# Performance work log

Hardware: AMD Instinct MI355X
Metric: run time of the kernel (lower is better)

## Reference

```python
import jax, jax.numpy as jnp
import numpy as np

N = 10000
E = 640000


def setup_inputs() -> dict:
    key = jax.random.key(0)
    k = jax.random.split(key, 6)
    x = jax.random.normal(k[0], (N, 128), dtype=jnp.float32)
    edge_index = jax.random.randint(k[1], (2, E), 0, N, dtype=jnp.int64)
    # Linear weights stored as [in, out] (torch stores [out, in]; math is x @ W.T + b)
    w1 = jax.random.normal(k[2], (128, 128), dtype=jnp.float32) * 0.05
    b1 = jax.random.normal(k[3], (128,), dtype=jnp.float32) * 0.05
    w2 = jax.random.normal(k[4], (128, 128), dtype=jnp.float32) * 0.05
    b2 = jax.random.normal(k[5], (128,), dtype=jnp.float32) * 0.05
    return {"x": x, "edge_index": edge_index, "w1": w1, "b1": b1, "w2": w2, "b2": b2}


def gin_conv(x, src, dst, w, b, eps=0.0):
    # aggregate: out[i] = sum over edges (src->dst=i) of x[src]
    agg = jax.ops.segment_sum(x[src], dst, num_segments=N)  # [N, d]
    h = (1.0 + eps) * x + agg
    return h @ w + b


def reference(x, edge_index, w1, b1, w2, b2):
    src, dst = edge_index[0], edge_index[1]
    h = gin_conv(x, src, dst, w1, b1)
    h = jax.nn.relu(h)
    h = gin_conv(h, src, dst, w2, b2)
    return jax.nn.log_softmax(h, axis=1)
```

## Files before the change

### kernel.cpp

```cpp
#include <hip/hip_runtime.h>
#include <cstdint>

#define NNODES 10000
#define FDIM 128
#define MAXDEG 192
#define SLOTS 48

typedef _Float16 h2v  __attribute__((ext_vector_type(2)));
typedef _Float16 f16x8 __attribute__((ext_vector_type(8)));
typedef float    f32x4 __attribute__((ext_vector_type(4)));

__device__ __align__(16)  int      g_cnt[NNODES * 4];
__device__                int      g_bucket[NNODES * MAXDEG];
__device__ __align__(256) unsigned g_xh [(NNODES + 1) * FDIM / 2];
__device__ __align__(256) unsigned g_h1h[(NNODES + 1) * FDIM / 2];
__device__ __align__(16)  unsigned g_wf[2 * 8192];

__device__ inline h2v as_h2(unsigned u) { return __builtin_bit_cast(h2v, u); }
__device__ inline unsigned as_u(h2v v) { return __builtin_bit_cast(unsigned, v); }
__device__ inline unsigned pack_f16x2(float a, float b) {
  h2v v; v[0] = (_Float16)a; v[1] = (_Float16)b;
  return as_u(v);
}
__device__ inline void vadd4(uint4& a, const uint4& b) {
  a.x = as_u(as_h2(a.x) + as_h2(b.x));
  a.y = as_u(as_h2(a.y) + as_h2(b.y));
  a.z = as_u(as_h2(a.z) + as_h2(b.z));
  a.w = as_u(as_h2(a.w) + as_h2(b.w));
}

__global__ __launch_bounds__(256) void prep_kernel(
    const float* __restrict__ x, const int* __restrict__ ei,
    const float* __restrict__ w1, const float* __restrict__ w2,
    int E_, int EBLK, int CBLK) {
  const int bid = blockIdx.x;
  if (bid < EBLK) {
    int e = bid * 256 + threadIdx.x;
    if (e < E_) {
      int d = ei[E_ + e];
      int s = ei[e];
      int st = e & 3;
      int p = atomicAdd(&g_cnt[d * 4 + st], 1);
      if (p < SLOTS) g_bucket[d * MAXDEG + st * SLOTS + p] = s;
    }
  } else if (bid < EBLK + CBLK) {
    int i = (bid - EBLK) * 256 + threadIdx.x;
    if (i < NNODES * 32) {
      float4 v = *(const float4*)(x + 4 * (size_t)i);
      uint2 o; o.x = pack_f16x2(v.x, v.y); o.y = pack_f16x2(v.z, v.w);
      *(uint2*)(g_xh + 2 * (size_t)i) = o;
    }
  } else {
    int idx = (bid - EBLK - CBLK) * 256 + threadIdx.x;
    const float* w = (idx >= 2048) ? w2 : w1;
    int s = idx & 2047;
    int sl = s & 63, nk = s >> 6;
    int n = nk >> 2, kc = nk & 3;
    int kbase = kc * 32 + (sl >> 4) * 8;
    int f = n * 16 + (sl & 15);
    unsigned d0 = pack_f16x2(w[(size_t)(kbase + 0) * FDIM + f],
                             w[(size_t)(kbase + 1) * FDIM + f]);
    unsigned d1 = pack_f16x2(w[(size_t)(kbase + 2) * FDIM + f],
                             w[(size_t)(kbase + 3) * FDIM + f]);
    unsigned d2 = pack_f16x2(w[(size_t)(kbase + 4) * FDIM + f],
                             w[(size_t)(kbase + 5) * FDIM + f]);
    unsigned d3 = pack_f16x2(w[(size_t)(kbase + 6) * FDIM + f],
                             w[(size_t)(kbase + 7) * FDIM + f]);
    *(uint4*)(g_wf + (idx >> 11) * 8192 + 4 * s) = make_uint4(d0, d1, d2, d3);
  }
}

template <int MODE>
__global__ __launch_bounds__(512) void gin_layer_kernel(
    const float* __restrict__ bvec,
    float* __restrict__ out_g) {
  const unsigned* __restrict__ xh = (MODE == 0) ? g_xh : g_h1h;

  __shared__ __align__(16) unsigned al[16 * 68];
  __shared__ __align__(16) unsigned cfu[8 * 132];

  const int tid = threadIdx.x;
  const int wave = tid >> 6, lane = tid & 63;
  const int quad = lane >> 4, m16 = lane & 15;
  const int node0 = blockIdx.x * 8;
  const int myn = node0 + wave;

  uint4 bf[4];
  {
    const unsigned* wfp = g_wf + (MODE ? 8192 : 0);
#pragma unroll
    for (int kc = 0; kc < 4; ++kc)
      bf[kc] = *(const uint4*)(wfp + ((wave * 4 + kc) * 64 + lane) * 4);
  }
  const float bb = bvec[wave * 16 + m16];

  for (int i2 = tid; i2 < 8 * 68; i2 += 512) al[8 * 68 + i2] = 0;

  uint4 self4 = *(const uint4*)(xh + (size_t)myn * 64 + (m16 << 2));
  int o1, o2, o3, deg;
  {
    int4 c = *(const int4*)(g_cnt + myn * 4);
    int a = (c.x > SLOTS) ? SLOTS : c.x;
    int bq = (c.y > SLOTS) ? SLOTS : c.y;
    int cq = (c.z > SLOTS) ? SLOTS : c.z;
    int dq = (c.w > SLOTS) ? SLOTS : c.w;
    o1 = a; o2 = a + bq; o3 = a + bq + cq; deg = a + bq + cq + dq;
  }

  const int* nb = g_bucket + (size_t)myn * MAXDEG;
  int idxr[3];
#pragma unroll
  for (int r = 0; r < 3; ++r) {
    int g = r * 64 + lane;
    int e = NNODES;
    if (g < deg) {
      int base = 0;
      if (g >= o1) base = o1;
      if (g >= o2) base = o2;
      if (g >= o3) base = o3;
      int st = (g >= o1) + (g >= o2) + (g >= o3);
      e = nb[st * SLOTS + (g - base)];
    }
    idxr[r] = e;
  }

  h2v a0 = as_h2(0u), a1 = as_h2(0u), a2 = as_h2(0u), a3 = as_h2(0u);
  const int nbat = (deg + 31) >> 5;
  for (int bt = 0; bt < nbat; ++bt) {
    const int s0 = bt << 3;
    const int r = s0 >> 4;
    const int src = (r == 0) ? idxr[0] : ((r == 1) ? idxr[1] : idxr[2]);
    uint4 t[8];
#pragma unroll
    for (int k = 0; k < 8; ++k) {
      int e = __builtin_amdgcn_ds_bpermute(
          (((((s0 + k) & 15) << 2) | quad) << 2), src);
      t[k] = *(const uint4*)(xh + (unsigned)((e << 6) | (m16 << 2)));
    }
#pragma unroll
    for (int st2 = 1; st2 < 8; st2 <<= 1)
#pragma unroll
      for (int k = 0; k < 8; k += 2 * st2) vadd4(t[k], t[k + st2]);
    a0 += as_h2(t[0].x); a1 += as_h2(t[0].y);
    a2 += as_h2(t[0].z); a3 += as_h2(t[0].w);
  }

  int rr;
  rr = __shfl_xor((int)as_u(a0), 16, 64); a0 += as_h2((unsigned)rr);
  rr = __shfl_xor((int)as_u(a0), 32, 64); a0 += as_h2((unsigned)rr);
  rr = __shfl_xor((int)as_u(a1), 16, 64); a1 += as_h2((unsigned)rr);
  rr = __shfl_xor((int)as_u(a1), 32, 64); a1 += as_h2((unsigned)rr);
  rr = __shfl_xor((int)as_u(a2), 16, 64); a2 += as_h2((unsigned)rr);
  rr = __shfl_xor((int)as_u(a2), 32, 64); a2 += as_h2((unsigned)rr);
  rr = __shfl_xor((int)as_u(a3), 16, 64); a3 += as_h2((unsigned)rr);
  rr = __shfl_xor((int)as_u(a3), 32, 64); a3 += as_h2((unsigned)rr);
  a0 += as_h2(self4.x); a1 += as_h2(self4.y);
  a2 += as_h2(self4.z); a3 += as_h2(self4.w);
  if (quad == 0)
    *(uint4*)(al + wave * 68 + (m16 << 2)) =
        make_uint4(as_u(a0), as_u(a1), as_u(a2), as_u(a3));
  __syncthreads();

  uint4 af[4];
#pragma unroll
  for (int kc = 0; kc < 4; ++kc)
    af[kc] = *(const uint4*)(al + m16 * 68 + kc * 16 + quad * 4);

  const int n = wave;
  f32x4 acc = {0.f, 0.f, 0.f, 0.f};
#pragma unroll
  for (int kc = 0; kc < 4; ++kc)
    acc = __builtin_amdgcn_mfma_f32_16x16x32_f16(
            __builtin_bit_cast(f16x8, af[kc]),
            __builtin_bit_cast(f16x8, bf[kc]), acc, 0, 0, 0);

  if (MODE == 0) {
    _Float16* ch = (_Float16*)cfu;
    const int f = n * 16 + m16;
    if (quad < 2) {
#pragma unroll
      for (int reg = 0; reg < 4; ++reg)
        ch[(quad * 4 + reg) * 136 + f] = (_Float16)fmaxf(acc[reg] + bb, 0.f);
    }
    __syncthreads();
    if (tid < 256) {
      const int row = tid >> 5, c2 = (tid & 31) * 2;
      uint2 v = *(const uint2*)(cfu + row * 68 + c2);
      *(uint2*)(&g_h1h[(size_t)(node0 + row) * 64 + c2]) = v;
    }
  } else {
    float* cf = (float*)cfu;
    const int f = n * 16 + m16;
    if (quad < 2) {
#pragma unroll
      for (int reg = 0; reg < 4; ++reg)
        cf[(quad * 4 + reg) * 132 + f] = acc[reg] + bb;
    }
    __syncthreads();
    if (tid < 256) {
      const int row = tid >> 5, li = tid & 31;
      const float* base = cf + row * 132 + li * 4;
      float4 a4 = *(const float4*)(base);
      float mx = fmaxf(fmaxf(a4.x, a4.y), fmaxf(a4.z, a4.w));
#pragma unroll
      for (int off = 16; off >= 1; off >>= 1)
        mx = fmaxf(mx, __shfl_xor(mx, off, 64));
      float s = (__expf(a4.x - mx) + __expf(a4.y - mx))
              + (__expf(a4.z - mx) + __expf(a4.w - mx));
#pragma unroll
      for (int off = 16; off >= 1; off >>= 1)
        s += __shfl_xor(s, off, 64);
      const float ls = mx + __logf(s);
      float* orow = out_g + (size_t)(node0 + row) * FDIM + li * 4;
      *(float4*)(orow) = make_float4(a4.x - ls, a4.y - ls, a4.z - ls, a4.w - ls);
    }
    if (tid < 32) g_cnt[node0 * 4 + tid] = 0;
  }
}

extern "C" void kernel_launch(void* const* d_in, const int* in_sizes, int n_in,
                              void* d_out, int out_size, void* d_ws, size_t ws_size,
                              hipStream_t stream) {
  const float* x  = (const float*)d_in[0];
  const int*   ei = (const int*)d_in[1];
  const float* w1 = (const float*)d_in[2];
  const float* b1 = (const float*)d_in[3];
  const float* w2 = (const float*)d_in[4];
  const float* b2 = (const float*)d_in[5];
  float* out = (float*)d_out;

  const int E_ = in_sizes[1] / 2;
  const int EBLK = (E_ + 255) / 256;
  const int CBLK = (NNODES * 32 + 255) / 256;
  const int WBLK = 16;

  prep_kernel<<<EBLK + CBLK + WBLK, 256, 0, stream>>>(x, ei, w1, w2, E_, EBLK, CBLK);

  gin_layer_kernel<0><<<1250, 512, 0, stream>>>(b1, nullptr);
  gin_layer_kernel<1><<<1250, 512, 0, stream>>>(b2, out);
}
```

Before: 124.2 us.

## Use one wave per 8-node block and pad counter stride to reduce atomic contention

New measurement: 142.1 us. +14.4%, slower.

```diff
diff --git a/kernel.cpp b/kernel.cpp
--- a/kernel.cpp
+++ b/kernel.cpp
@@ -5,12 +5,13 @@
 #define FDIM 128
 #define MAXDEG 192
 #define SLOTS 48
+#define CSTRIDE 16
 
 typedef _Float16 h2v  __attribute__((ext_vector_type(2)));
 typedef _Float16 f16x8 __attribute__((ext_vector_type(8)));
 typedef float    f32x4 __attribute__((ext_vector_type(4)));
 
-__device__ __align__(16)  int      g_cnt[NNODES * 4];
+__device__ __align__(16)  int      g_cnt[NNODES * CSTRIDE];
 __device__                int      g_bucket[NNODES * MAXDEG];
 __device__ __align__(256) unsigned g_xh [(NNODES + 1) * FDIM / 2];
 __device__ __align__(256) unsigned g_h1h[(NNODES + 1) * FDIM / 2];
@@ -40,7 +41,7 @@
       int d = ei[E_ + e];
       int s = ei[e];
       int st = e & 3;
-      int p = atomicAdd(&g_cnt[d * 4 + st], 1);
+      int p = atomicAdd(&g_cnt[d * CSTRIDE + st], 1);
       if (p < SLOTS) g_bucket[d * MAXDEG + st * SLOTS + p] = s;
     }
   } else if (bid < EBLK + CBLK) {
@@ -71,150 +72,179 @@
 }
 
 template <int MODE>
-__global__ __launch_bounds__(512) void gin_layer_kernel(
+__global__ __launch_bounds__(64) void gin_layer_kernel(
     const float* __restrict__ bvec,
     float* __restrict__ out_g) {
   const unsigned* __restrict__ xh = (MODE == 0) ? g_xh : g_h1h;
 
-  __shared__ __align__(16) unsigned al[16 * 68];
-  __shared__ __align__(16) unsigned cfu[8 * 132];
-
-  const int tid = threadIdx.x;
-  const int wave = tid >> 6, lane = tid & 63;
+  __shared__ __align__(16) unsigned buf[16 * 68];
+
+  const int lane = threadIdx.x;
   const int quad = lane >> 4, m16 = lane & 15;
   const int node0 = blockIdx.x * 8;
-  const int myn = node0 + wave;
-
-  uint4 bf[4];
-  {
-    const unsigned* wfp = g_wf + (MODE ? 8192 : 0);
-#pragma unroll
-    for (int kc = 0; kc < 4; ++kc)
-      bf[kc] = *(const uint4*)(wfp + ((wave * 4 + kc) * 64 + lane) * 4);
-  }
-  const float bb = bvec[wave * 16 + m16];
-
-  for (int i2 = tid; i2 < 8 * 68; i2 += 512) al[8 * 68 + i2] = 0;
-
-  uint4 self4 = *(const uint4*)(xh + (size_t)myn * 64 + (m16 << 2));
-  int o1, o2, o3, deg;
-  {
-    int4 c = *(const int4*)(g_cnt + myn * 4);
+
+  for (int i2 = lane; i2 < 8 * 68; i2 += 64) buf[8 * 68 + i2] = 0;
+
+  int4 cnxt = *(const int4*)(g_cnt + (size_t)node0 * CSTRIDE);
+  for (int nd = 0; nd < 8; ++nd) {
+    const int myn = node0 + nd;
+    int4 c = cnxt;
+    if (nd < 7)
+      cnxt = *(const int4*)(g_cnt + (size_t)(myn + 1) * CSTRIDE);
     int a = (c.x > SLOTS) ? SLOTS : c.x;
     int bq = (c.y > SLOTS) ? SLOTS : c.y;
     int cq = (c.z > SLOTS) ? SLOTS : c.z;
     int dq = (c.w > SLOTS) ? SLOTS : c.w;
-    o1 = a; o2 = a + bq; o3 = a + bq + cq; deg = a + bq + cq + dq;
-  }
-
-  const int* nb = g_bucket + (size_t)myn * MAXDEG;
-  int idxr[3];
-#pragma unroll
-  for (int r = 0; r < 3; ++r) {
-    int g = r * 64 + lane;
-    int e = NNODES;
-    if (g < deg) {
-      int base = 0;
-      if (g >= o1) base = o1;
-      if (g >= o2) base = o2;
-      if (g >= o3) base = o3;
-      int st = (g >= o1) + (g >= o2) + (g >= o3);
-      e = nb[st * SLOTS + (g - base)];
-    }
-    idxr[r] = e;
-  }
-
-  h2v a0 = as_h2(0u), a1 = as_h2(0u), a2 = as_h2(0u), a3 = as_h2(0u);
-  const int nbat = (deg + 31) >> 5;
-  for (int bt = 0; bt < nbat; ++bt) {
-    const int s0 = bt << 3;
-    const int r = s0 >> 4;
-    const int src = (r == 0) ? idxr[0] : ((r == 1) ? idxr[1] : idxr[2]);
-    uint4 t[8];
-#pragma unroll
-    for (int k = 0; k < 8; ++k) {
-      int e = __builtin_amdgcn_ds_bpermute(
-          (((((s0 + k) & 15) << 2) | quad) << 2), src);
-      t[k] = *(const uint4*)(xh + (unsigned)((e << 6) | (m16 << 2)));
-    }
-#pragma unroll
-    for (int st2 = 1; st2 < 8; st2 <<= 1)
-#pragma unroll
-      for (int k = 0; k < 8; k += 2 * st2) vadd4(t[k], t[k + st2]);
-    a0 += as_h2(t[0].x); a1 += as_h2(t[0].y);
-    a2 += as_h2(t[0].z); a3 += as_h2(t[0].w);
-  }
-
-  int rr;
-  rr = __shfl_xor((int)as_u(a0), 16, 64); a0 += as_h2((unsigned)rr);
-  rr = __shfl_xor((int)as_u(a0), 32, 64); a0 += as_h2((unsigned)rr);
-  rr = __shfl_xor((int)as_u(a1), 16, 64); a1 += as_h2((unsigned)rr);
-  rr = __shfl_xor((int)as_u(a1), 32, 64); a1 += as_h2((unsigned)rr);
-  rr = __shfl_xor((int)as_u(a2), 16, 64); a2 += as_h2((unsigned)rr);
-  rr = __shfl_xor((int)as_u(a2), 32, 64); a2 += as_h2((unsigned)rr);
-  rr = __shfl_xor((int)as_u(a3), 16, 64); a3 += as_h2((unsigned)rr);
-  rr = __shfl_xor((int)as_u(a3), 32, 64); a3 += as_h2((unsigned)rr);
-  a0 += as_h2(self4.x); a1 += as_h2(self4.y);
-  a2 += as_h2(self4.z); a3 += as_h2(self4.w);
-  if (quad == 0)
-    *(uint4*)(al + wave * 68 + (m16 << 2)) =
-        make_uint4(as_u(a0), as_u(a1), as_u(a2), as_u(a3));
+    const int o1 = a, o2 = a + bq, o3 = a + bq + cq;
+    const int deg = a + bq + cq + dq;
+
+    const int* nb = g_bucket + (size_t)myn * MAXDEG;
+    int i0 = NNODES, i1 = NNODES, i2r = NNODES;
+    {
+      int g = lane;
+      if (g < deg) {
+        int base = 0;
+        if (g >= o1) base = o1;
+        if (g >= o2) base = o2;
+        if (g >= o3) base = o3;
+        int st = (g >= o1) + (g >= o2) + (g >= o3);
+        i0 = nb[st * SLOTS + (g - base)];
+      }
+      g = 64 + lane;
+      if (g < deg) {
+        int base = 0;
+        if (g >= o1) base = o1;
+        if (g >= o2) base = o2;
+        if (g >= o3) base = o3;
+        int st = (g >= o1) + (g >= o2) + (g >= o3);
+        i1 = nb[st * SLOTS + (g - base)];
+      }
+      g = 128 + lane;
+      if (g < deg) {
+        int base = 0;
+        if (g >= o1) base = o1;
+        if (g >= o2) base = o2;
+        if (g >= o3) base = o3;
+        int st = (g >= o1) + (g >= o2) + (g >= o3);
+        i2r = nb[st * SLOTS + (g - base)];
+      }
+    }
+
+    uint4 self4 = *(const uint4*)(xh + (size_t)myn * 64 + (m16 << 2));
+
+    h2v a0 = as_h2(0u), a1 = as_h2(0u), a2 = as_h2(0u), a3 = as_h2(0u);
+    const int nbat = (deg + 31) >> 5;
+    for (int bt = 0; bt < nbat; ++bt) {
+      const int r = bt >> 1;
+      const int src = (r == 0) ? i0 : ((r == 1) ? i1 : i2r);
+      const int base = (bt & 1) << 5;
+      uint4 t[8];
+#pragma unroll
+      for (int k = 0; k < 8; ++k) {
+        int e = __builtin_amdgcn_ds_bpermute((base + 4 * k + quad) << 2, src);
+        t[k] = *(const uint4*)(xh + (unsigned)((e << 6) | (m16 << 2)));
+      }
+#pragma unroll
+      for (int st2 = 1; st2 < 8; st2 <<= 1)
+#pragma unroll
+        for (int k = 0; k < 8; k += 2 * st2) vadd4(t[k], t[k + st2]);
+      a0 += as_h2(t[0].x); a1 += as_h2(t[0].y);
+      a2 += as_h2(t[0].z); a3 += as_h2(t[0].w);
+    }
+
+    int rr;
+    rr = __shfl_xor((int)as_u(a0), 16, 64); a0 += as_h2((unsigned)rr);
+    rr = __shfl_xor((int)as_u(a0), 32, 64); a0 += as_h2((unsigned)rr);
+    rr = __shfl_xor((int)as_u(a1), 16, 64); a1 += as_h2((unsigned)rr);
+    rr = __shfl_xor((int)as_u(a1), 32, 64); a1 += as_h2((unsigned)rr);
+    rr = __shfl_xor((int)as_u(a2), 16, 64); a2 += as_h2((unsigned)rr);
+    rr = __shfl_xor((int)as_u(a2), 32, 64); a2 += as_h2((unsigned)rr);
+    rr = __shfl_xor((int)as_u(a3), 16, 64); a3 += as_h2((unsigned)rr);
+    rr = __shfl_xor((int)as_u(a3), 32, 64); a3 += as_h2((unsigned)rr);
+    a0 += as_h2(self4.x); a1 += as_h2(self4.y);
+    a2 += as_h2(self4.z); a3 += as_h2(self4.w);
+    if (quad == 0)
+      *(uint4*)(buf + nd * 68 + (m16 << 2)) =
+          make_uint4(as_u(a0), as_u(a1), as_u(a2), as_u(a3));
+  }
   __syncthreads();
 
   uint4 af[4];
 #pragma unroll
   for (int kc = 0; kc < 4; ++kc)
-    af[kc] = *(const uint4*)(al + m16 * 68 + kc * 16 + quad * 4);
-
-  const int n = wave;
-  f32x4 acc = {0.f, 0.f, 0.f, 0.f};
-#pragma unroll
-  for (int kc = 0; kc < 4; ++kc)
-    acc = __builtin_amdgcn_mfma_f32_16x16x32_f16(
-            __builtin_bit_cast(f16x8, af[kc]),
-            __builtin_bit_cast(f16x8, bf[kc]), acc, 0, 0, 0);
+    af[kc] = *(const uint4*)(buf + m16 * 68 + kc * 16 + quad * 4);
+  __syncthreads();
+
+  const unsigned* wfp = g_wf + (MODE ? 8192 : 0);
+#pragma unroll
+  for (int n = 0; n < 8; ++n) {
+    f32x4 acc = {0.f, 0.f, 0.f, 0.f};
+#pragma unroll
+    for (int kc = 0; kc < 4; ++kc) {
+      uint4 bfr = *(const uint4*)(wfp + ((n * 4 + kc) * 64 + lane) * 4);
+      acc = __builtin_amdgcn_mfma_f32_16x16x32_f16(
+              __builtin_bit_cast(f16x8, af[kc]),
+              __builtin_bit_cast(f16x8, bfr), acc, 0, 0, 0);
+    }
+    const float bbn = bvec[n * 16 + m16];
+    if (MODE == 0) {
+      _Float16* ch = (_Float16*)buf;
+      const int f = n * 16 + m16;
+      if (quad < 2) {
+#pragma unroll
+        for (int reg = 0; reg < 4; ++reg)
+          ch[(quad * 4 + reg) * 136 + f] = (_Float16)fmaxf(acc[reg] + bbn, 0.f);
+      }
+    } else {
+      float* cf = (float*)buf;
+      const int f = n * 16 + m16;
+      if (quad < 2) {
+#pragma unroll
+        for (int reg = 0; reg < 4; ++reg)
+          cf[(quad * 4 + reg) * 132 + f] = acc[reg] + bbn;
+      }
+    }
+  }
+  __syncthreads();
 
   if (MODE == 0) {
-    _Float16* ch = (_Float16*)cfu;
-    const int f = n * 16 + m16;
-    if (quad < 2) {
-#pragma unroll
-      for (int reg = 0; reg < 4; ++reg)
-        ch[(quad * 4 + reg) * 136 + f] = (_Float16)fmaxf(acc[reg] + bb, 0.f);
-    }
-    __syncthreads();
-    if (tid < 256) {
-      const int row = tid >> 5, c2 = (tid & 31) * 2;
-      uint2 v = *(const uint2*)(cfu + row * 68 + c2);
+    const int row = lane >> 3;
+#pragma unroll
+    for (int j = 0; j < 4; ++j) {
+      const int c2 = (lane & 7) * 2 + j * 16;
+      uint2 v = *(const uint2*)(buf + row * 68 + c2);
       *(uint2*)(&g_h1h[(size_t)(node0 + row) * 64 + c2]) = v;
     }
   } else {
-    float* cf = (float*)cfu;
-    const int f = n * 16 + m16;
-    if (quad < 2) {
-#pragma unroll
-      for (int reg = 0; reg < 4; ++reg)
-        cf[(quad * 4 + reg) * 132 + f] = acc[reg] + bb;
-    }
-    __syncthreads();
-    if (tid < 256) {
-      const int row = tid >> 5, li = tid & 31;
-      const float* base = cf + row * 132 + li * 4;
-      float4 a4 = *(const float4*)(base);
-      float mx = fmaxf(fmaxf(a4.x, a4.y), fmaxf(a4.z, a4.w));
-#pragma unroll
-      for (int off = 16; off >= 1; off >>= 1)
-        mx = fmaxf(mx, __shfl_xor(mx, off, 64));
-      float s = (__expf(a4.x - mx) + __expf(a4.y - mx))
-              + (__expf(a4.z - mx) + __expf(a4.w - mx));
-#pragma unroll
-      for (int off = 16; off >= 1; off >>= 1)
-        s += __shfl_xor(s, off, 64);
-      const float ls = mx + __logf(s);
-      float* orow = out_g + (size_t)(node0 + row) * FDIM + li * 4;
-      *(float4*)(orow) = make_float4(a4.x - ls, a4.y - ls, a4.z - ls, a4.w - ls);
-    }
-    if (tid < 32) g_cnt[node0 * 4 + tid] = 0;
+    const float* cf = (const float*)buf;
+    const int row = lane >> 3, li = lane & 7;
+    const float* base = cf + row * 132 + li * 16;
+    float4 v[4];
+#pragma unroll
+    for (int jj = 0; jj < 4; ++jj) v[jj] = *(const float4*)(base + jj * 4);
+    float mx = -1e30f;
+#pragma unroll
+    for (int jj = 0; jj < 4; ++jj)
+      mx = fmaxf(mx, fmaxf(fmaxf(v[jj].x, v[jj].y), fmaxf(v[jj].z, v[jj].w)));
+#pragma unroll
+    for (int off = 4; off >= 1; off >>= 1)
+      mx = fmaxf(mx, __shfl_xor(mx, off, 64));
+    float s = 0.f;
+#pragma unroll
+    for (int jj = 0; jj < 4; ++jj)
+      s += (__expf(v[jj].x - mx) + __expf(v[jj].y - mx))
+         + (__expf(v[jj].z - mx) + __expf(v[jj].w - mx));
+#pragma unroll
+    for (int off = 4; off >= 1; off >>= 1)
+      s += __shfl_xor(s, off, 64);
+    const float ls = mx + __logf(s);
+    float* orow = out_g + (size_t)(node0 + row) * FDIM + li * 16;
+#pragma unroll
+    for (int jj = 0; jj < 4; ++jj)
+      *(float4*)(orow + jj * 4) =
+          make_float4(v[jj].x - ls, v[jj].y - ls, v[jj].z - ls, v[jj].w - ls);
+    if (lane < 32)
+      g_cnt[(node0 + (lane >> 2)) * CSTRIDE + (lane & 3)] = 0;
   }
 }
 
@@ -236,6 +266,6 @@
 
   prep_kernel<<<EBLK + CBLK + WBLK, 256, 0, stream>>>(x, ei, w1, w2, E_, EBLK, CBLK);
 
-  gin_layer_kernel<0><<<1250, 512, 0, stream>>>(b1, nullptr);
-  gin_layer_kernel<1><<<1250, 512, 0, stream>>>(b2, out);
-}
+  gin_layer_kernel<0><<<1250, 64, 0, stream>>>(b1, nullptr);
+  gin_layer_kernel<1><<<1250, 64, 0, stream>>>(b2, out);
+}
```

## Build adjacency buckets in shared memory per node range with 16-bit indices

Applied to the files above, without the earlier changes.

New measurement: 397.1 us. +219.7%, slower.

```diff
diff --git a/kernel.cpp b/kernel.cpp
--- a/kernel.cpp
+++ b/kernel.cpp
@@ -4,14 +4,15 @@
 #define NNODES 10000
 #define FDIM 128
 #define MAXDEG 192
-#define SLOTS 48
+#define NPB 157
+#define SCANBLK 64
 
 typedef _Float16 h2v  __attribute__((ext_vector_type(2)));
 typedef _Float16 f16x8 __attribute__((ext_vector_type(8)));
 typedef float    f32x4 __attribute__((ext_vector_type(4)));
 
-__device__ __align__(16)  int      g_cnt[NNODES * 4];
-__device__                int      g_bucket[NNODES * MAXDEG];
+__device__ __align__(16)  int            g_cnt[NNODES];
+__device__ __align__(16)  unsigned short g_bkt[NNODES * MAXDEG];
 __device__ __align__(256) unsigned g_xh [(NNODES + 1) * FDIM / 2];
 __device__ __align__(256) unsigned g_h1h[(NNODES + 1) * FDIM / 2];
 __device__ __align__(16)  unsigned g_wf[2 * 8192];
@@ -29,44 +30,73 @@
   a.w = as_u(as_h2(a.w) + as_h2(b.w));
 }
 
-__global__ __launch_bounds__(256) void prep_kernel(
+__global__ __launch_bounds__(512) void prep_kernel(
     const float* __restrict__ x, const int* __restrict__ ei,
     const float* __restrict__ w1, const float* __restrict__ w2,
-    int E_, int EBLK, int CBLK) {
-  const int bid = blockIdx.x;
-  if (bid < EBLK) {
-    int e = bid * 256 + threadIdx.x;
-    if (e < E_) {
-      int d = ei[E_ + e];
-      int s = ei[e];
-      int st = e & 3;
-      int p = atomicAdd(&g_cnt[d * 4 + st], 1);
-      if (p < SLOTS) g_bucket[d * MAXDEG + st * SLOTS + p] = s;
-    }
-  } else if (bid < EBLK + CBLK) {
-    int i = (bid - EBLK) * 256 + threadIdx.x;
+    int E_) {
+  __shared__ int lcnt[NPB];
+  __shared__ __align__(16) unsigned short lbkt[NPB * MAXDEG];
+
+  const int bid = blockIdx.x, tid = threadIdx.x;
+  if (bid < SCANBLK) {
+    const int lo = bid * NPB;
+    const int nn = (NNODES - lo < NPB) ? (NNODES - lo) : NPB;
+    for (int i = tid; i < NPB; i += 512) lcnt[i] = 0;
+    __syncthreads();
+
+    const int iters = (E_ + 511) >> 9;
+    for (int it = 0; it < iters; it += 8) {
+      int dv[8];
+#pragma unroll
+      for (int k = 0; k < 8; ++k) {
+        int e = (it + k) * 512 + tid;
+        dv[k] = (e < E_) ? ei[E_ + e] : -1;
+      }
+#pragma unroll
+      for (int k = 0; k < 8; ++k) {
+        unsigned rel = (unsigned)(dv[k] - lo);
+        if (rel < (unsigned)nn) {
+          int e = (it + k) * 512 + tid;
+          int s = ei[e];
+          int p = atomicAdd(&lcnt[rel], 1);
+          if (p < MAXDEG) lbkt[rel * MAXDEG + p] = (unsigned short)s;
+        }
+      }
+    }
+    __syncthreads();
+
+    for (int i = tid; i < nn; i += 512)
+      g_cnt[lo + i] = (lcnt[i] > MAXDEG) ? MAXDEG : lcnt[i];
+    const int nq = nn * (MAXDEG * 2 / 16);
+    const uint4* srcq = (const uint4*)lbkt;
+    uint4* dstq = (uint4*)(g_bkt + (size_t)lo * MAXDEG);
+    for (int i = tid; i < nq; i += 512) dstq[i] = srcq[i];
+  } else if (bid < SCANBLK + 625) {
+    int i = (bid - SCANBLK) * 512 + tid;
     if (i < NNODES * 32) {
       float4 v = *(const float4*)(x + 4 * (size_t)i);
       uint2 o; o.x = pack_f16x2(v.x, v.y); o.y = pack_f16x2(v.z, v.w);
       *(uint2*)(g_xh + 2 * (size_t)i) = o;
     }
   } else {
-    int idx = (bid - EBLK - CBLK) * 256 + threadIdx.x;
-    const float* w = (idx >= 2048) ? w2 : w1;
-    int s = idx & 2047;
-    int sl = s & 63, nk = s >> 6;
-    int n = nk >> 2, kc = nk & 3;
-    int kbase = kc * 32 + (sl >> 4) * 8;
-    int f = n * 16 + (sl & 15);
-    unsigned d0 = pack_f16x2(w[(size_t)(kbase + 0) * FDIM + f],
-                             w[(size_t)(kbase + 1) * FDIM + f]);
-    unsigned d1 = pack_f16x2(w[(size_t)(kbase + 2) * FDIM + f],
-                             w[(size_t)(kbase + 3) * FDIM + f]);
-    unsigned d2 = pack_f16x2(w[(size_t)(kbase + 4) * FDIM + f],
-                             w[(size_t)(kbase + 5) * FDIM + f]);
-    unsigned d3 = pack_f16x2(w[(size_t)(kbase + 6) * FDIM + f],
-                             w[(size_t)(kbase + 7) * FDIM + f]);
-    *(uint4*)(g_wf + (idx >> 11) * 8192 + 4 * s) = make_uint4(d0, d1, d2, d3);
+    int idx = (bid - SCANBLK - 625) * 512 + tid;
+    if (idx < 4096) {
+      const float* w = (idx >= 2048) ? w2 : w1;
+      int s = idx & 2047;
+      int sl = s & 63, nk = s >> 6;
+      int n = nk >> 2, kc = nk & 3;
+      int kbase = kc * 32 + (sl >> 4) * 8;
+      int f = n * 16 + (sl & 15);
+      unsigned d0 = pack_f16x2(w[(size_t)(kbase + 0) * FDIM + f],
+                               w[(size_t)(kbase + 1) * FDIM + f]);
+      unsigned d1 = pack_f16x2(w[(size_t)(kbase + 2) * FDIM + f],
+                               w[(size_t)(kbase + 3) * FDIM + f]);
+      unsigned d2 = pack_f16x2(w[(size_t)(kbase + 4) * FDIM + f],
+                               w[(size_t)(kbase + 5) * FDIM + f]);
+      unsigned d3 = pack_f16x2(w[(size_t)(kbase + 6) * FDIM + f],
+                               w[(size_t)(kbase + 7) * FDIM + f]);
+      *(uint4*)(g_wf + (idx >> 11) * 8192 + 4 * s) = make_uint4(d0, d1, d2, d3);
+    }
   }
 }
 
@@ -97,44 +127,26 @@
   for (int i2 = tid; i2 < 8 * 68; i2 += 512) al[8 * 68 + i2] = 0;
 
   uint4 self4 = *(const uint4*)(xh + (size_t)myn * 64 + (m16 << 2));
-  int o1, o2, o3, deg;
-  {
-    int4 c = *(const int4*)(g_cnt + myn * 4);
-    int a = (c.x > SLOTS) ? SLOTS : c.x;
-    int bq = (c.y > SLOTS) ? SLOTS : c.y;
-    int cq = (c.z > SLOTS) ? SLOTS : c.z;
-    int dq = (c.w > SLOTS) ? SLOTS : c.w;
-    o1 = a; o2 = a + bq; o3 = a + bq + cq; deg = a + bq + cq + dq;
-  }
-
-  const int* nb = g_bucket + (size_t)myn * MAXDEG;
+  const int deg = g_cnt[myn];
+
+  const unsigned short* nb16 = g_bkt + (size_t)myn * MAXDEG;
   int idxr[3];
 #pragma unroll
   for (int r = 0; r < 3; ++r) {
     int g = r * 64 + lane;
-    int e = NNODES;
-    if (g < deg) {
-      int base = 0;
-      if (g >= o1) base = o1;
-      if (g >= o2) base = o2;
-      if (g >= o3) base = o3;
-      int st = (g >= o1) + (g >= o2) + (g >= o3);
-      e = nb[st * SLOTS + (g - base)];
-    }
-    idxr[r] = e;
+    idxr[r] = (g < deg) ? (int)nb16[g] : NNODES;
   }
 
   h2v a0 = as_h2(0u), a1 = as_h2(0u), a2 = as_h2(0u), a3 = as_h2(0u);
   const int nbat = (deg + 31) >> 5;
   for (int bt = 0; bt < nbat; ++bt) {
-    const int s0 = bt << 3;
-    const int r = s0 >> 4;
+    const int r = bt >> 1;
     const int src = (r == 0) ? idxr[0] : ((r == 1) ? idxr[1] : idxr[2]);
+    const int base = (bt & 1) << 5;
     uint4 t[8];
 #pragma unroll
     for (int k = 0; k < 8; ++k) {
-      int e = __builtin_amdgcn_ds_bpermute(
-          (((((s0 + k) & 15) << 2) | quad) << 2), src);
+      int e = __builtin_amdgcn_ds_bpermute((base + 4 * k + quad) << 2, src);
       t[k] = *(const uint4*)(xh + (unsigned)((e << 6) | (m16 << 2)));
     }
 #pragma unroll
@@ -214,7 +226,6 @@
       float* orow = out_g + (size_t)(node0 + row) * FDIM + li * 4;
       *(float4*)(orow) = make_float4(a4.x - ls, a4.y - ls, a4.z - ls, a4.w - ls);
     }
-    if (tid < 32) g_cnt[node0 * 4 + tid] = 0;
   }
 }
 
@@ -230,11 +241,8 @@
   float* out = (float*)d_out;
 
   const int E_ = in_sizes[1] / 2;
-  const int EBLK = (E_ + 255) / 256;
-  const int CBLK = (NNODES * 32 + 255) / 256;
-  const int WBLK = 16;
-
-  prep_kernel<<<EBLK + CBLK + WBLK, 256, 0, stream>>>(x, ei, w1, w2, E_, EBLK, CBLK);
+
+  prep_kernel<<<SCANBLK + 625 + 8, 512, 0, stream>>>(x, ei, w1, w2, E_);
 
   gin_layer_kernel<0><<<1250, 512, 0, stream>>>(b1, nullptr);
   gin_layer_kernel<1><<<1250, 512, 0, stream>>>(b2, out);
```
